# Performance work log

Measured on AMD Instinct MI355X. Metric: run time of the kernel, lower is better.

The kernel has to match this reference:

```python
import jax, jax.numpy as jnp
import numpy as np

FP8_MAX = 448.0  # e4m3fn saturation value

def q8(x):
    """Round-to-nearest-even quantization to float8 e4m3fn values (kept in fp32).
    Normal min exponent -6, mantissa 3 bits, subnormal step 2^-9, saturate at 448."""
    a = jnp.abs(x)
    e = jnp.clip(jnp.floor(jnp.log2(jnp.maximum(a, 1e-30))), -6.0, 8.0)
    step = jnp.exp2(e - 3.0)  # mantissa quantization step for this binade
    q = jnp.minimum(jnp.round(a / step) * step, FP8_MAX)  # jnp.round is half-to-even
    return jnp.sign(x) * q

def setup_inputs() -> dict:
    key = jax.random.key(0)
    k1, k2, k3 = jax.random.split(key, 3)
    B, D_IN, D_H, D_OUT = 8192, 1024, 4096, 1024
    x = jax.random.normal(k1, (B, D_IN), jnp.float32)
    # learned weights (torch Linear layout: [out, in]); scaled to a realistic FP8 range
    w1 = jax.random.normal(k2, (D_H, D_IN), jnp.float32) * 0.03
    w2 = jax.random.normal(k3, (D_OUT, D_H), jnp.float32) * 0.03
    return {"x": x, "w1": w1, "w2": w2}

def reference(x, w1, w2):
    # x -> fp8 e4m3fn -> bit-pulse encode (lossless round trip for fp8 values)
    x8 = q8(x)
    # spike FP8 linear layers carry fp8 weights (set_weight_from_float quantizes)
    w1q = q8(w1)
    w2q = q8(w2)
    # fc1: spike spatial-encoding adder == accumulate wide, emit FP8 pulses
    h = q8(jnp.einsum('bi,hi->bh', x8, w1q))
    # SpikeFP8ReLU: zero out negative fp8 pulse values
    h = jnp.where(h > 0, h, 0.0)
    # fc2 then fp8_bits_to_float decode
    out = q8(jnp.einsum('bh,oh->bo', h, w2q))
    return out
```

## Files before the change

### kernel.cpp

```cpp
#include <hip/hip_runtime.h>
#include <stdint.h>
#include <stddef.h>

typedef int v4i __attribute__((ext_vector_type(4)));

#define SROW 1040
#define KCH  1024
#define LDSB (128 * SROW)

__device__ __forceinline__ void gl_lds16(const uint8_t* g, uint8_t* l) {
    __builtin_amdgcn_global_load_lds(
        (const __attribute__((address_space(1))) uint32_t*)g,
        (__attribute__((address_space(3))) uint32_t*)l,
        16, 0, 0);
}

__device__ __forceinline__ float q8f(float v) {
    float a = fabsf(v);
    int e = (int)(__float_as_uint(a) >> 23) - 127;
    e = e < -6 ? -6 : (e > 8 ? 8 : e);
    float step  = __uint_as_float((uint32_t)(e - 3 + 127) << 23);
    float rstep = __uint_as_float((uint32_t)(3 - e + 127) << 23);
    float q = fminf(rintf(a * rstep) * step, 448.0f);
    return v < 0.0f ? -q : q;
}

__device__ __forceinline__ int qm(float v) {
    return (int)rintf(q8f(v) * 512.0f);
}

__global__ __launch_bounds__(256) void quant_x_kernel(
    const float* __restrict__ in, uint32_t* __restrict__ xh, uint32_t* __restrict__ xl, int n4) {
    int i = blockIdx.x * 256 + threadIdx.x;
    if (i >= n4) return;
    float4 v = ((const float4*)in)[i];
    int m0 = qm(v.x), m1 = qm(v.y), m2 = qm(v.z), m3 = qm(v.w);
    xh[i] = ((uint32_t)((m0 >> 5) & 0xff)) | ((uint32_t)((m1 >> 5) & 0xff) << 8) |
            ((uint32_t)((m2 >> 5) & 0xff) << 16) | ((uint32_t)((m3 >> 5) & 0xff) << 24);
    xl[i] = ((uint32_t)(m0 & 31)) | ((uint32_t)(m1 & 31) << 8) |
            ((uint32_t)(m2 & 31) << 16) | ((uint32_t)(m3 & 31) << 24);
}

__global__ __launch_bounds__(256) void quant_w_kernel(
    const float* __restrict__ in, uint32_t* __restrict__ wm, int n4) {
    int i = blockIdx.x * 256 + threadIdx.x;
    if (i >= n4) return;
    float4 v = ((const float4*)in)[i];
    wm[i] = ((uint32_t)(qm(v.x) & 0xff)) | ((uint32_t)(qm(v.y) & 0xff) << 8) |
            ((uint32_t)(qm(v.z) & 0xff) << 16) | ((uint32_t)(qm(v.w) & 0xff) << 24);
}

template <int EPI>
__global__ __launch_bounds__(512, 2) void gemm_i8_big(
    const uint8_t* __restrict__ Ah, const uint8_t* __restrict__ Al,
    const uint8_t* __restrict__ Bm,
    void* __restrict__ Ch, void* __restrict__ Cl,
    int M, int N, int K) {
    extern __shared__ uint8_t sB[];

    const int tid  = threadIdx.x;
    const int lane = tid & 63;
    const int wave = tid >> 6;
    const int q    = lane >> 4;
    const int rr   = lane & 15;
    const int bm = blockIdx.x, bn = blockIdx.y;

    v4i acc[2][2][8];
#pragma unroll
    for (int p = 0; p < 2; ++p)
#pragma unroll
        for (int i = 0; i < 2; ++i)
#pragma unroll
            for (int j = 0; j < 8; ++j) acc[p][i][j] = (v4i){0, 0, 0, 0};

    const uint8_t* pA[2][2];
#pragma unroll
    for (int i = 0; i < 2; ++i) {
        size_t row = (size_t)(bm * 256 + wave * 32 + i * 16 + rr);
        pA[0][i] = Ah + row * K + q * 16;
        pA[1][i] = Al + row * K + q * 16;
    }
    int bbase[8];
#pragma unroll
    for (int j = 0; j < 8; ++j) bbase[j] = (j * 16 + rr) * SROW + q * 16;

    for (int kc = 0; kc < K; kc += KCH) {
        if (kc) __syncthreads();
        {
            const size_t go = (size_t)(bn * 128 + wave) * K + kc + lane * 16;
            uint8_t* lo = sB + wave * SROW + lane * 16;
            for (int c = 0; c < 16; ++c)
                gl_lds16(Bm + go + (size_t)c * 8 * K, lo + c * 8 * SROW);
        }
        __syncthreads();

#pragma unroll 4
        for (int k0 = 0; k0 < KCH; k0 += 64) {
            v4i a[2][2], b[8];
#pragma unroll
            for (int i = 0; i < 2; ++i) {
                a[0][i] = *(const v4i*)(pA[0][i] + kc + k0);
                a[1][i] = *(const v4i*)(pA[1][i] + kc + k0);
            }
#pragma unroll
            for (int j = 0; j < 8; ++j)
                b[j] = *(const v4i*)(sB + bbase[j] + k0);
#pragma unroll
            for (int i = 0; i < 2; ++i)
#pragma unroll
                for (int j = 0; j < 8; ++j) {
                    acc[0][i][j] = __builtin_amdgcn_mfma_i32_16x16x64_i8(a[0][i], b[j], acc[0][i][j], 0, 0, 0);
                    acc[1][i][j] = __builtin_amdgcn_mfma_i32_16x16x64_i8(a[1][i], b[j], acc[1][i][j], 0, 0, 0);
                }
        }
    }

    const int c0 = bn * 128 + rr;
    const int r0 = bm * 256 + wave * 32 + q * 4;
#pragma unroll
    for (int i = 0; i < 2; ++i) {
#pragma unroll
        for (int j = 0; j < 8; ++j) {
#pragma unroll
            for (int r = 0; r < 4; ++r) {
                int mt = acc[0][i][j][r] * 32 + acc[1][i][j][r];
                float sum = (float)mt * 0x1p-18f;
                float qv = q8f(sum);
                size_t idx = (size_t)(r0 + i * 16 + r) * N + (size_t)(c0 + j * 16);
                if (EPI == 0) {
                    int m = (qv > 0.0f) ? (int)rintf(qv * 512.0f) : 0;
                    ((uint8_t*)Ch)[idx] = (uint8_t)(m >> 5);
                    ((uint8_t*)Cl)[idx] = (uint8_t)(m & 31);
                } else {
                    ((float*)Ch)[idx] = qv;
                }
            }
        }
    }
}

extern "C" void kernel_launch(void* const* d_in, const int* in_sizes, int n_in,
                              void* d_out, int out_size, void* d_ws, size_t ws_size,
                              hipStream_t stream) {
    const int Bsz = 8192, DIN = 1024, DH = 4096, DOUT = 1024;
    const float* x  = (const float*)d_in[0];
    const float* w1 = (const float*)d_in[1];
    const float* w2 = (const float*)d_in[2];
    float* out = (float*)d_out;

    uint8_t* ws  = (uint8_t*)d_ws;
    uint8_t* xh  = ws;
    uint8_t* xl  = xh  + (size_t)Bsz * DIN;
    uint8_t* w1m = xl  + (size_t)Bsz * DIN;
    uint8_t* w2m = w1m + (size_t)DH  * DIN;
    uint8_t* hh  = w2m + (size_t)DOUT * DH;
    uint8_t* hl  = hh  + (size_t)Bsz * DH;

    static bool attr_done = false;
    if (!attr_done) {
        hipFuncSetAttribute((const void*)gemm_i8_big<0>,
                            hipFuncAttributeMaxDynamicSharedMemorySize, LDSB);
        hipFuncSetAttribute((const void*)gemm_i8_big<1>,
                            hipFuncAttributeMaxDynamicSharedMemorySize, LDSB);
        attr_done = true;
    }

    quant_x_kernel<<<(Bsz * DIN / 4) / 256, 256, 0, stream>>>(
        x, (uint32_t*)xh, (uint32_t*)xl, Bsz * DIN / 4);
    quant_w_kernel<<<(DH * DIN / 4) / 256, 256, 0, stream>>>(
        w1, (uint32_t*)w1m, DH * DIN / 4);
    quant_w_kernel<<<(DOUT * DH / 4) / 256, 256, 0, stream>>>(
        w2, (uint32_t*)w2m, DOUT * DH / 4);

    dim3 g1(Bsz / 256, DH / 128);
    gemm_i8_big<0><<<g1, 512, LDSB, stream>>>(xh, xl, w1m, (void*)hh, (void*)hl, Bsz, DH, DIN);

    dim3 g2(Bsz / 256, DOUT / 128);
    gemm_i8_big<1><<<g2, 512, LDSB, stream>>>(hh, hl, w2m, (void*)out, nullptr, Bsz, DOUT, DH);
}
```

Baseline: 270.5 us.

## Double-buffer B tiles in LDS and switch to 32x32x32 int8 MFMA

```diff
diff --git a/kernel.cpp b/kernel.cpp
--- a/kernel.cpp
+++ b/kernel.cpp
@@ -2,11 +2,13 @@
 #include <stdint.h>
 #include <stddef.h>
 
-typedef int v4i __attribute__((ext_vector_type(4)));
-
-#define SROW 1040
-#define KCH  1024
-#define LDSB (128 * SROW)
+typedef int v4i  __attribute__((ext_vector_type(4)));
+typedef int v16i __attribute__((ext_vector_type(16)));
+
+#define KCH  512
+#define PSTR 1040
+#define BUFB (64 * PSTR)
+#define LDSB (2 * BUFB)
 
 __device__ __forceinline__ void gl_lds16(const uint8_t* g, uint8_t* l) {
     __builtin_amdgcn_global_load_lds(
@@ -24,9 +26,16 @@
     float q = fminf(rintf(a * rstep) * step, 448.0f);
     return v < 0.0f ? -q : q;
 }
-
 __device__ __forceinline__ int qm(float v) {
     return (int)rintf(q8f(v) * 512.0f);
+}
+
+__device__ __forceinline__ uint32_t rne_sh(uint32_t a, int s) {
+    uint32_t t = a >> s;
+    uint32_t rem = a & ((1u << s) - 1u);
+    uint32_t half = 1u << (s - 1);
+    t += (rem > half) || (rem == half && (t & 1u));
+    return t;
 }
 
 __global__ __launch_bounds__(256) void quant_x_kernel(
@@ -61,79 +70,92 @@
     const int tid  = threadIdx.x;
     const int lane = tid & 63;
     const int wave = tid >> 6;
-    const int q    = lane >> 4;
-    const int rr   = lane & 15;
+    const int col  = lane & 31;
+    const int kh   = lane >> 5;
     const int bm = blockIdx.x, bn = blockIdx.y;
 
-    v4i acc[2][2][8];
+    v16i acc[2][4];
 #pragma unroll
     for (int p = 0; p < 2; ++p)
 #pragma unroll
-        for (int i = 0; i < 2; ++i)
-#pragma unroll
-            for (int j = 0; j < 8; ++j) acc[p][i][j] = (v4i){0, 0, 0, 0};
-
-    const uint8_t* pA[2][2];
-#pragma unroll
-    for (int i = 0; i < 2; ++i) {
-        size_t row = (size_t)(bm * 256 + wave * 32 + i * 16 + rr);
-        pA[0][i] = Ah + row * K + q * 16;
-        pA[1][i] = Al + row * K + q * 16;
-    }
-    int bbase[8];
-#pragma unroll
-    for (int j = 0; j < 8; ++j) bbase[j] = (j * 16 + rr) * SROW + q * 16;
-
-    for (int kc = 0; kc < K; kc += KCH) {
-        if (kc) __syncthreads();
-        {
-            const size_t go = (size_t)(bn * 128 + wave) * K + kc + lane * 16;
-            uint8_t* lo = sB + wave * SROW + lane * 16;
-            for (int c = 0; c < 16; ++c)
-                gl_lds16(Bm + go + (size_t)c * 8 * K, lo + c * 8 * SROW);
+        for (int j = 0; j < 4; ++j) acc[p][j] = (v16i)0;
+
+    const size_t arow = (size_t)(bm * 256 + wave * 32 + col);
+    const uint8_t* pAh = Ah + arow * K + kh * 16;
+    const uint8_t* pAl = Al + arow * K + kh * 16;
+
+    const size_t brow = (size_t)(bn * 128 + wave * 16 + kh);
+    int bbase[4];
+#pragma unroll
+    for (int j = 0; j < 4; ++j)
+        bbase[j] = (j * 16 + (col >> 1)) * PSTR + (col & 1) * 512 + kh * 16;
+
+    const int NC = K / KCH;
+    {
+        const uint8_t* g = Bm + brow * K + (lane & 31) * 16;
+        uint8_t* l = sB + wave * 8 * PSTR + lane * 16;
+#pragma unroll
+        for (int c = 0; c < 8; ++c)
+            gl_lds16(g + (size_t)(2 * c) * K, l + c * PSTR);
+    }
+
+    for (int c = 0; c < NC; ++c) {
+        __syncthreads();
+        if (c + 1 < NC) {
+            const uint8_t* g = Bm + brow * K + (c + 1) * KCH + (lane & 31) * 16;
+            uint8_t* l = sB + ((c + 1) & 1) * BUFB + wave * 8 * PSTR + lane * 16;
+#pragma unroll
+            for (int s = 0; s < 8; ++s)
+                gl_lds16(g + (size_t)(2 * s) * K, l + s * PSTR);
         }
-        __syncthreads();
-
+        const uint8_t* bufc = sB + (c & 1) * BUFB;
+        const int kc = c * KCH;
 #pragma unroll 4
-        for (int k0 = 0; k0 < KCH; k0 += 64) {
-            v4i a[2][2], b[8];
-#pragma unroll
-            for (int i = 0; i < 2; ++i) {
-                a[0][i] = *(const v4i*)(pA[0][i] + kc + k0);
-                a[1][i] = *(const v4i*)(pA[1][i] + kc + k0);
+        for (int k0 = 0; k0 < KCH; k0 += 32) {
+            v4i a0 = *(const v4i*)(pAh + kc + k0);
+            v4i a1 = *(const v4i*)(pAl + kc + k0);
+            v4i b[4];
+#pragma unroll
+            for (int j = 0; j < 4; ++j)
+                b[j] = *(const v4i*)(bufc + bbase[j] + k0);
+#pragma unroll
+            for (int j = 0; j < 4; ++j) {
+                acc[0][j] = __builtin_amdgcn_mfma_i32_32x32x32_i8(a0, b[j], acc[0][j], 0, 0, 0);
+                acc[1][j] = __builtin_amdgcn_mfma_i32_32x32x32_i8(a1, b[j], acc[1][j], 0, 0, 0);
             }
-#pragma unroll
-            for (int j = 0; j < 8; ++j)
-                b[j] = *(const v4i*)(sB + bbase[j] + k0);
-#pragma unroll
-            for (int i = 0; i < 2; ++i)
-#pragma unroll
-                for (int j = 0; j < 8; ++j) {
-                    acc[0][i][j] = __builtin_amdgcn_mfma_i32_16x16x64_i8(a[0][i], b[j], acc[0][i][j], 0, 0, 0);
-                    acc[1][i][j] = __builtin_amdgcn_mfma_i32_16x16x64_i8(a[1][i], b[j], acc[1][i][j], 0, 0, 0);
+        }
+    }
+
+    const int cg0 = bn * 128 + col;
+    const int rg0 = bm * 256 + wave * 32 + 4 * kh;
+#pragma unroll
+    for (int j = 0; j < 4; ++j) {
+#pragma unroll
+        for (int reg = 0; reg < 16; ++reg) {
+            int mt = acc[0][j][reg] * 32 + acc[1][j][reg];
+            size_t idx = (size_t)(rg0 + (reg & 3) + 8 * (reg >> 2)) * N
+                       + (size_t)(cg0 + j * 32);
+            if (EPI == 0) {
+                uint8_t hb = 0, lb = 0;
+                if (mt > 0) {
+                    int s = 28 - __builtin_clz((uint32_t)mt);
+                    if (s < 9) s = 9;
+                    int mh = (int)(rne_sh((uint32_t)mt, s) << (s - 9));
+                    hb = (uint8_t)(mh >> 5);
+                    lb = (uint8_t)(mh & 31);
                 }
-        }
-    }
-
-    const int c0 = bn * 128 + rr;
-    const int r0 = bm * 256 + wave * 32 + q * 4;
-#pragma unroll
-    for (int i = 0; i < 2; ++i) {
-#pragma unroll
-        for (int j = 0; j < 8; ++j) {
-#pragma unroll
-            for (int r = 0; r < 4; ++r) {
-                int mt = acc[0][i][j][r] * 32 + acc[1][i][j][r];
-                float sum = (float)mt * 0x1p-18f;
-                float qv = q8f(sum);
-                size_t idx = (size_t)(r0 + i * 16 + r) * N + (size_t)(c0 + j * 16);
-                if (EPI == 0) {
-                    int m = (qv > 0.0f) ? (int)rintf(qv * 512.0f) : 0;
-                    ((uint8_t*)Ch)[idx] = (uint8_t)(m >> 5);
-                    ((uint8_t*)Cl)[idx] = (uint8_t)(m & 31);
-                } else {
-                    ((float*)Ch)[idx] = qv;
+                ((uint8_t*)Ch)[idx] = hb;
+                ((uint8_t*)Cl)[idx] = lb;
+            } else {
+                uint32_t a = mt < 0 ? (uint32_t)(-mt) : (uint32_t)mt;
+                float v = 0.0f;
+                if (a) {
+                    int s = 28 - __builtin_clz(a);
+                    if (s < 9) s = 9;
+                    v = (float)(rne_sh(a, s) << s) * 0x1p-18f;
+                    if (mt < 0) v = -v;
                 }
+                ((float*)Ch)[idx] = v;
             }
         }
     }
```

Result: slower. 293.2 us (+8.4%).
